# Kernel optimization log

Hardware: AMD Instinct MI355X
Metric: run time of the kernel (lower is better)

The kernel has to match this reference:

```python
import jax, jax.numpy as jnp
import numpy as np

B, N, NFEAT, NHID, NHEADS, NBLK = 8, 512, 32, 128, 4, 6


def _lrelu(x):
    return jax.nn.leaky_relu(x, 0.01)


def _layernorm(x, eps=1e-5):
    m = jnp.mean(x, axis=-1, keepdims=True)
    v = jnp.mean((x - m) ** 2, axis=-1, keepdims=True)
    return (x - m) / jnp.sqrt(v + eps)


def _gat(x, W, a, mask, concat):
    # x:[b,n,f]  W:[H,f,o]  a:[H,2o]  mask:[b,n,n] bool
    o = W.shape[-1]
    Wh = jnp.einsum('bnf,hfo->hbno', x, W)
    s1 = jnp.einsum('hbno,ho->hbn', Wh, a[:, :o])   # Wh @ a[:o]
    s2 = jnp.einsum('hbno,ho->hbn', Wh, a[:, o:])   # Wh @ a[o:]
    # rank-1 score: e[i,j] = leakyrelu(s1[i]*s2[j])
    e = _lrelu(s1[:, :, :, None] * s2[:, :, None, :])  # [h,b,n,n]
    e = jnp.where(mask[None], e, jnp.float32(-9e15))
    att = jax.nn.softmax(e, axis=-1)
    att = jnp.where(mask[None], att, jnp.float32(0.0))
    hp = jnp.einsum('hbij,hbjo->hbio', att, Wh)
    return jax.nn.elu(hp) if concat else hp


def _attn_block(x, W, a, rW, rb, mask):
    res = x
    h = _gat(x, W, a, mask, True)                      # [H,b,n,o]
    h = jnp.moveaxis(h, 0, 2).reshape(x.shape[0], x.shape[1], -1)  # concat heads
    h = h @ rW + rb
    if h.shape[-1] == res.shape[-1]:
        h = h + res
    return _layernorm(h)


def _fel(x, f1w1, f1b1, f1w2, f1b2, f2w1, f2b1, f2w2, f2b2, f3w1, f3b1, f3w2, f3b2):
    res = _lrelu(_lrelu(x @ f1w1 + f1b1) @ f1w2 + f1b2)
    h = _lrelu(_lrelu(res @ f2w1 + f2b1) @ f2w2 + f2b2)
    x = _layernorm(h + res)
    res = x
    h = _lrelu(res @ f3w1 + f3b1) @ f3w2 + f3b2
    return _layernorm(h + res)


def setup_inputs() -> dict:
    key = jax.random.key(0)
    ks = iter(jax.random.split(key, 24))
    nrm = lambda shape: jax.random.normal(next(ks), shape, jnp.float32) * 0.05
    inp = {}
    inp['x'] = jax.random.normal(next(ks), (B, N, NFEAT), jnp.float32)
    inp['adj'] = jax.random.randint(next(ks), (B, N, N), 0, 2, jnp.int32)
    inp['layer_id'] = 0
    inp['f1w1'] = nrm((NFEAT, NHID)); inp['f1b1'] = jnp.zeros((NHID,), jnp.float32)
    inp['f1w2'] = nrm((NHID, NHID)); inp['f1b2'] = jnp.zeros((NHID,), jnp.float32)
    inp['f2w1'] = nrm((NHID, 2 * NHID)); inp['f2b1'] = jnp.zeros((2 * NHID,), jnp.float32)
    inp['f2w2'] = nrm((2 * NHID, NHID)); inp['f2b2'] = jnp.zeros((NHID,), jnp.float32)
    inp['f3w1'] = nrm((NHID, 2 * NHID)); inp['f3b1'] = jnp.zeros((2 * NHID,), jnp.float32)
    inp['f3w2'] = nrm((2 * NHID, NHID)); inp['f3b2'] = jnp.zeros((NHID,), jnp.float32)
    inp['att_W'] = nrm((NBLK, NHEADS, NHID, NHID))
    inp['att_a'] = nrm((NBLK, NHEADS, 2 * NHID))
    inp['resh_W'] = nrm((NBLK, NHEADS * NHID, NHID))
    inp['resh_b'] = jnp.zeros((NBLK, NHID), jnp.float32)
    inp['out_W'] = nrm((2, NHID, NHID))
    inp['out_a'] = nrm((2, 2 * NHID))
    inp['proj_W'] = nrm((2 * NHID, 1))
    inp['proj_b'] = jnp.zeros((1,), jnp.float32)
    return inp


def reference(x, adj, layer_id, f1w1, f1b1, f1w2, f1b2, f2w1, f2b1, f2w2, f2b2,
              f3w1, f3b1, f3w2, f3b2, att_W, att_a, resh_W, resh_b, out_W, out_a,
              proj_W, proj_b):
    mask = adj > 0
    mask_t = jnp.transpose(adj, (0, 2, 1)) > 0
    h = _fel(x, f1w1, f1b1, f1w2, f1b2, f2w1, f2b1, f2w2, f2b2, f3w1, f3b1, f3w2, f3b2)
    for i in range(3):
        h = _attn_block(h, att_W[i], att_a[i], resh_W[i], resh_b[i], mask)
    h = _lrelu(_gat(h, out_W[0:1], out_a[0:1], mask, False)[0])
    ht = h
    for i in range(3, 6):
        ht = _attn_block(ht, att_W[i], att_a[i], resh_W[i], resh_b[i], mask_t)
    ht = _lrelu(_gat(ht, out_W[1:2], out_a[1:2], mask_t, False)[0])
    z = jnp.concatenate([h, ht], axis=-1)   # [b,n,2*nhid]
    z = jnp.mean(z, axis=1)                 # sum/length
    return jnp.squeeze(z @ proj_W + proj_b, axis=1)
```

## Files before the change

kernel.cpp:

```cpp
#include <hip/hip_runtime.h>
#include <math.h>

#define B 8
#define N 512
#define D 128
#define H 4
#define TOK (B*N)

typedef __attribute__((ext_vector_type(8))) short bfrag;
typedef __attribute__((ext_vector_type(4))) float facc;
typedef unsigned short u16;
typedef unsigned int u32;

__device__ __forceinline__ float lrelu(float x){ return x > 0.f ? x : 0.01f*x; }
__device__ __forceinline__ u16 f2bf(float f){
  u32 u = __float_as_uint(f);
  u += 0x7fffu + ((u >> 16) & 1u);
  return (u16)(u >> 16);
}
__device__ __forceinline__ u32 pk2(float a, float b){
  return (u32)f2bf(a) | ((u32)f2bf(b) << 16);
}

#define LS 72

__global__ void prep_kernel(const int* __restrict__ adj,
    u32* __restrict__ mbits, u32* __restrict__ mtbits,
    const float* s0, const float* s1_, const float* s2_, const float* s3,
    const float* s4, const float* s5, const float* s6, const float* s7,
    const float* s8,
    u16* d0, u16* d1, u16* d2, u16* d3, u16* d4, u16* d5, u16* d6, u16* d7, u16* d8)
{
  __shared__ float ftile[32][33];
  const int tid = threadIdx.x;
  const int tx = tid & 31, ty = tid >> 5;
  if (blockIdx.x < 128){
    int* it = (int*)&ftile[0][0];
    const int b = blockIdx.x >> 4, i0 = (blockIdx.x & 15)*32;
    const int lane6 = tid & 63;
    for (int j0 = 0; j0 < N; j0 += 32){
      for (int r = ty; r < 32; r += 8)
        it[r*33 + tx] = adj[((size_t)b*N + i0 + r)*N + j0 + tx];
      __syncthreads();
      #pragma unroll
      for (int half = 0; half < 4; ++half){
        const int r = half*8 + (tid >> 5);
        const int c = tid & 31;
        unsigned long long bl = __ballot(it[r*33 + c] > 0);
        if (lane6 == 0 || lane6 == 32)
          mbits[((size_t)b*N + i0 + r)*16 + (j0>>5)] = (u32)(lane6 ? (bl >> 32) : bl);
        unsigned long long bt = __ballot(it[c*33 + r] > 0);
        if (lane6 == 0 || lane6 == 32)
          mtbits[((size_t)b*N + j0 + r)*16 + (i0>>5)] = (u32)(lane6 ? (bt >> 32) : bt);
      }
      __syncthreads();
    }
  } else {
    const float* srcs[9] = {s0,s1_,s2_,s3,s4,s5,s6,s7,s8};
    u16* dsts[9] = {d0,d1,d2,d3,d4,d5,d6,d7,d8};
    const int Ks[9] = {32,128,128,256,128,256,128,128,512};
    const int Ns[9] = {128,128,256,128,256,128,128,128,128};
    const int zs[9] = {1,1,1,1,1,1,24,2,6};
    for (int job = (int)blockIdx.x - 128; job < 948; job += 384){
      int m = 0, base = 0;
      for (; m < 9; ++m){
        int cnt = (Ks[m]>>5)*(Ns[m]>>5)*zs[m];
        if (job < base + cnt) break;
        base += cnt;
      }
      const int rem = job - base;
      const int tn = Ns[m] >> 5;
      const int per = (Ks[m] >> 5)*tn;
      const int z = rem / per, t = rem % per;
      const int k0 = (t / tn)*32, n0 = (t % tn)*32;
      const float* src = srcs[m] + (size_t)z*Ks[m]*Ns[m];
      u16* dst = dsts[m] + (size_t)z*Ks[m]*Ns[m];
      __syncthreads();
      for (int r = ty; r < 32; r += 8)
        ftile[r][tx] = src[(size_t)(k0+r)*Ns[m] + n0 + tx];
      __syncthreads();
      for (int r = ty; r < 32; r += 8)
        dst[(size_t)(n0+r)*Ks[m] + k0 + tx] = f2bf(ftile[tx][r]);
    }
  }
}

__device__ __forceinline__ void stageB64(const u16* __restrict__ BTn, int ldb,
                                         int k0, u16* Bs, int tid){
  const int n = tid >> 1, part = tid & 1;
  const u16* wp = BTn + (size_t)n*ldb + k0 + part*32;
  uint4 w0 = *(const uint4*)wp,      w1 = *(const uint4*)(wp+8);
  uint4 w2 = *(const uint4*)(wp+16), w3 = *(const uint4*)(wp+24);
  *(uint4*)&Bs[n*LS + part*32]      = w0;
  *(uint4*)&Bs[n*LS + part*32 + 8]  = w1;
  *(uint4*)&Bs[n*LS + part*32 + 16] = w2;
  *(uint4*)&Bs[n*LS + part*32 + 24] = w3;
}
__device__ __forceinline__ void stageB32(const u16* __restrict__ BTn, int ldb,
                                         int k0, u16* Bs, int tid){
  const int n = tid >> 1, part = tid & 1;
  const u16* wp = BTn + (size_t)n*ldb + k0 + part*16;
  uint4 w0 = *(const uint4*)wp, w1 = *(const uint4*)(wp+8);
  *(uint4*)&Bs[n*LS + part*16]     = w0;
  *(uint4*)&Bs[n*LS + part*16 + 8] = w1;
}

__device__ __forceinline__ void mfma64(const u16* As, const u16* Bs,
                                       facc acc[4], int r0, int c0,
                                       int quad, int l15){
  #pragma unroll
  for (int kk = 0; kk < 2; ++kk){
    bfrag af = *(const bfrag*)&As[(r0 + l15)*LS + kk*32 + quad*8];
    #pragma unroll
    for (int g = 0; g < 4; ++g){
      bfrag bf = *(const bfrag*)&Bs[(c0 + g*16 + l15)*LS + kk*32 + quad*8];
      acc[g] = __builtin_amdgcn_mfma_f32_16x16x32_bf16(af, bf, acc[g], 0,0,0);
    }
  }
}
__device__ __forceinline__ void mfma32(const u16* As, const u16* Bs,
                                       facc acc[4], int r0, int c0,
                                       int quad, int l15){
  bfrag af = *(const bfrag*)&As[(r0 + l15)*LS + quad*8];
  #pragma unroll
  for (int g = 0; g < 4; ++g){
    bfrag bf = *(const bfrag*)&Bs[(c0 + g*16 + l15)*LS + quad*8];
    acc[g] = __builtin_amdgcn_mfma_f32_16x16x32_bf16(af, bf, acc[g], 0,0,0);
  }
}

__device__ __forceinline__ void mfma64w(const u16* As, const u16* Bs,
                                        facc acc[2][2], int c0,
                                        int quad, int l15){
  #pragma unroll
  for (int kk = 0; kk < 2; ++kk){
    bfrag af0 = *(const bfrag*)&As[(l15)*LS      + kk*32 + quad*8];
    bfrag af1 = *(const bfrag*)&As[(16 + l15)*LS + kk*32 + quad*8];
    #pragma unroll
    for (int f = 0; f < 2; ++f){
      bfrag bf = *(const bfrag*)&Bs[(c0 + f*16 + l15)*LS + kk*32 + quad*8];
      acc[0][f] = __builtin_amdgcn_mfma_f32_16x16x32_bf16(af0, bf, acc[0][f], 0,0,0);
      acc[1][f] = __builtin_amdgcn_mfma_f32_16x16x32_bf16(af1, bf, acc[1][f], 0,0,0);
    }
  }
}

template<int ACT, int FIN>
__global__ __launch_bounds__(256) void gemm32(
    const float* __restrict__ A, int lda, int K,
    const u16* __restrict__ BT, const float* __restrict__ bias,
    const float* __restrict__ res, float* __restrict__ out, int ldo)
{
  const int tid = threadIdx.x;
  const int t0 = blockIdx.x * 32;
  const int n0 = blockIdx.y * 128;
  __shared__ __align__(16) u16 As[32*LS];
  __shared__ __align__(16) u16 Bs[128*LS];
  __shared__ float scrS[4][16], scrQ[4][16];
  const int wave = tid >> 6, lane = tid & 63, quad = lane >> 4, l15 = lane & 15;
  const int r0 = (wave & 1)*16, c0 = (wave >> 1)*64;
  facc acc[4];
  #pragma unroll
  for (int g = 0; g < 4; ++g) acc[g] = (facc){0.f,0.f,0.f,0.f};
  const u16* BTn = BT + (size_t)n0*K;

  int k0 = 0;
  for (; k0 + 64 <= K; k0 += 64){
    { const int row = tid >> 3, ko = tid & 7;
      const float* ap = A + (size_t)(t0+row)*lda + k0 + ko*8;
      float4 a0 = *(const float4*)ap, a1 = *(const float4*)(ap+4);
      uint4 u = { pk2(a0.x,a0.y), pk2(a0.z,a0.w), pk2(a1.x,a1.y), pk2(a1.z,a1.w) };
      *(uint4*)&As[row*LS + ko*8] = u;
    }
    stageB64(BTn, K, k0, Bs, tid);
    __syncthreads();
    mfma64(As, Bs, acc, r0, c0, quad, l15);
    __syncthreads();
  }
  if (k0 < K){
    { const int row = tid >> 3, ko = tid & 7;
      float4 a0 = *(const float4*)(A + (size_t)(t0+row)*lda + k0 + ko*4);
      uint2 u = { pk2(a0.x,a0.y), pk2(a0.z,a0.w) };
      *(uint2*)&As[row*LS + ko*4] = u;
    }
    stageB32(BTn, K, k0, Bs, tid);
    __syncthreads();
    mfma32(As, Bs, acc, r0, c0, quad, l15);
    __syncthreads();
  }

  float bv[4];
  #pragma unroll
  for (int g = 0; g < 4; ++g) bv[g] = bias[n0 + c0 + g*16 + l15];

  if (FIN == 0){
    #pragma unroll
    for (int g = 0; g < 4; ++g){
      const int c = n0 + c0 + g*16 + l15;
      #pragma unroll
      for (int q = 0; q < 4; ++q){
        const int rq = t0 + r0 + quad*4 + q;
        float xv = acc[g][q] + bv[g];
        if (ACT) xv = lrelu(xv);
        out[(size_t)rq*ldo + c] = xv;
      }
    }
  } else {
    float v[4][4], s[4] = {0,0,0,0}, sq[4] = {0,0,0,0};
    #pragma unroll
    for (int g = 0; g < 4; ++g){
      const int c = c0 + g*16 + l15;
      #pragma unroll
      for (int q = 0; q < 4; ++q){
        const int rq = t0 + r0 + quad*4 + q;
        float xv = acc[g][q] + bv[g];
        if (ACT) xv = lrelu(xv);
        xv += res[(size_t)rq*128 + c];
        v[g][q] = xv; s[q] += xv; sq[q] += xv*xv;
      }
    }
    #pragma unroll
    for (int m = 1; m < 16; m <<= 1){
      #pragma unroll
      for (int q = 0; q < 4; ++q){ s[q] += __shfl_xor(s[q], m, 64); sq[q] += __shfl_xor(sq[q], m, 64); }
    }
    if (l15 == 0){
      #pragma unroll
      for (int q = 0; q < 4; ++q){ scrS[wave][quad*4+q] = s[q]; scrQ[wave][quad*4+q] = sq[q]; }
    }
    __syncthreads();
    #pragma unroll
    for (int q = 0; q < 4; ++q){
      const int rq = t0 + r0 + quad*4 + q;
      const float fs = s[q] + scrS[wave^2][quad*4+q];
      const float fq = sq[q] + scrQ[wave^2][quad*4+q];
      const float mean = fs*(1.f/D);
      const float rstd = rsqrtf(fq*(1.f/D) - mean*mean + 1e-5f);
      #pragma unroll
      for (int g = 0; g < 4; ++g)
        out[(size_t)rq*128 + c0 + g*16 + l15] = (v[g][q] - mean)*rstd;
    }
  }
}

__global__ __launch_bounds__(256) void gemm32b(
    const u16* __restrict__ A, int lda, int K,
    const u16* __restrict__ BT, const float* __restrict__ bias,
    const float* __restrict__ res, float* __restrict__ out)
{
  const int tid = threadIdx.x;
  const int t0 = blockIdx.x * 32;
  __shared__ __align__(16) u16 As[2][32*LS];
  __shared__ __align__(16) u16 Bs[2][128*LS];
  __shared__ float scrS[4][32], scrQ[4][32];
  const int wave = tid >> 6, lane = tid & 63, quad = lane >> 4, l15 = lane & 15;
  const int c0 = wave*32;
  facc acc[2][2];
  #pragma unroll
  for (int rg = 0; rg < 2; ++rg)
    #pragma unroll
    for (int f = 0; f < 2; ++f) acc[rg][f] = (facc){0.f,0.f,0.f,0.f};

  const int arow = tid >> 3, ako = tid & 7;
  const u16* aptr = A + (size_t)(t0+arow)*lda + ako*8;
  const int bn = tid >> 1, bpart = tid & 1;
  const u16* bptr = BT + (size_t)bn*K + bpart*32;

  { uint4 ga = *(const uint4*)aptr;
    uint4 g0 = *(const uint4*)bptr,      g1 = *(const uint4*)(bptr+8);
    uint4 g2 = *(const uint4*)(bptr+16), g3 = *(const uint4*)(bptr+24);
    *(uint4*)&As[0][arow*LS + ako*8] = ga;
    u16* bp = &Bs[0][bn*LS + bpart*32];
    *(uint4*)bp = g0; *(uint4*)(bp+8) = g1; *(uint4*)(bp+16) = g2; *(uint4*)(bp+24) = g3;
  }
  __syncthreads();

  const int nt = K >> 6;
  for (int k = 0; k < nt - 1; ++k){
    const int cur = k & 1, nxt = cur ^ 1;
    uint4 na = *(const uint4*)(aptr + (k+1)*64);
    const u16* wp = bptr + (k+1)*64;
    uint4 n0 = *(const uint4*)wp,      n1 = *(const uint4*)(wp+8);
    uint4 n2 = *(const uint4*)(wp+16), n3 = *(const uint4*)(wp+24);
    mfma64w(As[cur], Bs[cur], acc, c0, quad, l15);
    *(uint4*)&As[nxt][arow*LS + ako*8] = na;
    { u16* bp = &Bs[nxt][bn*LS + bpart*32];
      *(uint4*)bp = n0; *(uint4*)(bp+8) = n1; *(uint4*)(bp+16) = n2; *(uint4*)(bp+24) = n3; }
    __syncthreads();
  }
  mfma64w(As[(nt-1)&1], Bs[(nt-1)&1], acc, c0, quad, l15);

  float bv[2];
  #pragma unroll
  for (int f = 0; f < 2; ++f) bv[f] = bias[c0 + f*16 + l15];
  float v[2][2][4], s[2][4], sq[2][4];
  #pragma unroll
  for (int rg = 0; rg < 2; ++rg)
    #pragma unroll
    for (int q = 0; q < 4; ++q){ s[rg][q] = 0.f; sq[rg][q] = 0.f; }
  #pragma unroll
  for (int rg = 0; rg < 2; ++rg){
    #pragma unroll
    for (int f = 0; f < 2; ++f){
      const int c = c0 + f*16 + l15;
      #pragma unroll
      for (int q = 0; q < 4; ++q){
        const int rq = t0 + rg*16 + quad*4 + q;
        float xv = acc[rg][f][q] + bv[f] + res[(size_t)rq*128 + c];
        v[rg][f][q] = xv; s[rg][q] += xv; sq[rg][q] += xv*xv;
      }
    }
  }
  #pragma unroll
  for (int m = 1; m < 16; m <<= 1){
    #pragma unroll
    for (int rg = 0; rg < 2; ++rg)
      #pragma unroll
      for (int q = 0; q < 4; ++q){ s[rg][q] += __shfl_xor(s[rg][q], m, 64); sq[rg][q] += __shfl_xor(sq[rg][q], m, 64); }
  }
  if (l15 == 0){
    #pragma unroll
    for (int rg = 0; rg < 2; ++rg)
      #pragma unroll
      for (int q = 0; q < 4; ++q){
        scrS[wave][rg*16 + quad*4 + q] = s[rg][q];
        scrQ[wave][rg*16 + quad*4 + q] = sq[rg][q];
      }
  }
  __syncthreads();
  #pragma unroll
  for (int rg = 0; rg < 2; ++rg){
    #pragma unroll
    for (int q = 0; q < 4; ++q){
      const int row = rg*16 + quad*4 + q;
      const float fs = scrS[0][row] + scrS[1][row] + scrS[2][row] + scrS[3][row];
      const float fq = scrQ[0][row] + scrQ[1][row] + scrQ[2][row] + scrQ[3][row];
      const float mean = fs*(1.f/D);
      const float rstd = rsqrtf(fq*(1.f/D) - mean*mean + 1e-5f);
      #pragma unroll
      for (int f = 0; f < 2; ++f)
        out[(size_t)(t0+row)*128 + c0 + f*16 + l15] = (v[rg][f][q] - mean)*rstd;
    }
  }
}

__global__ __launch_bounds__(256) void wh32(
    const float* __restrict__ hin, const u16* __restrict__ WT,
    const float* __restrict__ a, u16* __restrict__ WhT,
    float* __restrict__ s1, float* __restrict__ s2)
{
  const int tid = threadIdx.x;
  const int h  = blockIdx.x >> 7;
  const int t0 = (blockIdx.x & 127) * 32;
  const int b = t0 >> 9, j0 = t0 & (N-1);
  __shared__ __align__(16) u16 As[32*LS];
  __shared__ __align__(16) u16 Bs[128*LS];
  __shared__ float r1s[2][32], r2s[2][32];
  const int wave = tid >> 6, lane = tid & 63, quad = lane >> 4, l15 = lane & 15;
  const int r0 = (wave & 1)*16, c0 = (wave >> 1)*64;
  facc acc[4];
  #pragma unroll
  for (int g = 0; g < 4; ++g) acc[g] = (facc){0.f,0.f,0.f,0.f};
  const u16* BTn = WT + (size_t)h*D*D;

  #pragma unroll
  for (int k0 = 0; k0 < D; k0 += 64){
    { const int row = tid >> 3, ko = tid & 7;
      const float* ap = hin + (size_t)(t0+row)*D + k0 + ko*8;
      float4 a0 = *(const float4*)ap, a1 = *(const float4*)(ap+4);
      uint4 u = { pk2(a0.x,a0.y), pk2(a0.z,a0.w), pk2(a1.x,a1.y), pk2(a1.z,a1.w) };
      *(uint4*)&As[row*LS + ko*8] = u;
    }
    stageB64(BTn, D, k0, Bs, tid);
    __syncthreads();
    mfma64(As, Bs, acc, r0, c0, quad, l15);
    __syncthreads();
  }

  const float* ah = a + (size_t)h*2*D;
  const size_t obase = (size_t)(h*8 + b)*128;
  float p1[4] = {0,0,0,0}, p2[4] = {0,0,0,0};
  #pragma unroll
  for (int g = 0; g < 4; ++g){
    const int c = c0 + g*16 + l15;
    const float a1v = ah[c], a2v = ah[D + c];
    ushort4 wv;
    wv.x = f2bf(acc[g][0]); wv.y = f2bf(acc[g][1]);
    wv.z = f2bf(acc[g][2]); wv.w = f2bf(acc[g][3]);
    *(ushort4*)&WhT[(obase + c)*N + j0 + r0 + quad*4] = wv;
    #pragma unroll
    for (int q = 0; q < 4; ++q){
      p1[q] = fmaf(acc[g][q], a1v, p1[q]);
      p2[q] = fmaf(acc[g][q], a2v, p2[q]);
    }
  }
  #pragma unroll
  for (int m = 1; m < 16; m <<= 1){
    #pragma unroll
    for (int q = 0; q < 4; ++q){ p1[q] += __shfl_xor(p1[q], m, 64); p2[q] += __shfl_xor(p2[q], m, 64); }
  }
  if (l15 == 0){
    #pragma unroll
    for (int q = 0; q < 4; ++q){
      r1s[wave>>1][r0 + quad*4 + q] = p1[q];
      r2s[wave>>1][r0 + quad*4 + q] = p2[q];
    }
  }
  __syncthreads();
  if (tid < 32){
    s1[(size_t)h*TOK + t0 + tid] = r1s[0][tid] + r1s[1][tid];
    s2[(size_t)h*TOK + t0 + tid] = r2s[0][tid] + r2s[1][tid];
  }
}

__device__ __forceinline__ float score8(const float* s2s, const unsigned char* mrow,
                                        float s1lr, int k0, int lq, u16* asp){
  float4 sa = *(const float4*)&s2s[k0 + lq*8];
  float4 sb = *(const float4*)&s2s[k0 + lq*8 + 4];
  const u32 mm = mrow[(k0 >> 3) + lq];
  float ss[8] = {sa.x,sa.y,sa.z,sa.w,sb.x,sb.y,sb.z,sb.w};
  float v[8]; float p = 0.f;
  #pragma unroll
  for (int i = 0; i < 8; ++i){
    float e = lrelu(s1lr * ss[i]);
    float ex = ((mm >> i) & 1u) ? __expf(e) : 0.f;
    v[i] = ex; p += ex;
  }
  uint4 u = { pk2(v[0],v[1]), pk2(v[2],v[3]), pk2(v[4],v[5]), pk2(v[6],v[7]) };
  *(uint4*)asp = u;
  return p;
}

template<int MODE, int OBF>
__global__ __launch_bounds__(256) void pv32(
    const float* __restrict__ s1, const float* __restrict__ s2,
    const u32* __restrict__ mbits, const u16* __restrict__ WhT,
    void* __restrict__ out_, int ldo, int hcs)
{
  const int tid = threadIdx.x;
  const int h  = blockIdx.x >> 7;
  const int t0 = (blockIdx.x & 127) * 32;
  const int b = t0 >> 9, i0 = t0 & (N-1);
  __shared__ float s2s[N];
  __shared__ float s1s[32], sums[32];
  __shared__ u32 mbs[32*16];
  __shared__ __align__(16) u16 As[2][32*LS];
  __shared__ __align__(16) u16 Bs[2][128*LS];

  s2s[tid]     = s2[(size_t)h*TOK + b*N + tid];
  s2s[tid+256] = s2[(size_t)h*TOK + b*N + tid + 256];
  if (tid < 32) s1s[tid] = s1[(size_t)h*TOK + t0 + tid];
  { const int r = tid >> 3, wd = (tid & 7)*2;
    *(uint2*)&mbs[r*16 + wd] = *(const uint2*)&mbits[((size_t)b*N + i0 + r)*16 + wd];
  }

  const u16* BTn = WhT + (size_t)(h*8 + b)*128*N;
  const int wave = tid >> 6, lane = tid & 63, quad = lane >> 4, l15 = lane & 15;
  const int c0 = wave*32;
  facc acc[2][2];
  #pragma unroll
  for (int rg = 0; rg < 2; ++rg)
    #pragma unroll
    for (int f = 0; f < 2; ++f) acc[rg][f] = (facc){0.f,0.f,0.f,0.f};

  const int lr = tid >> 3, lq = tid & 7;
  const unsigned char* mrow = (const unsigned char*)&mbs[lr*16];
  const int bn = tid >> 1, bpart = tid & 1;
  const u16* bwp = BTn + (size_t)bn*N + bpart*32;
  float psum = 0.f;

  uint4 g0 = *(const uint4*)bwp,      g1 = *(const uint4*)(bwp+8);
  uint4 g2 = *(const uint4*)(bwp+16), g3 = *(const uint4*)(bwp+24);
  __syncthreads();
  const float s1lr = s1s[lr];
  psum += score8(s2s, mrow, s1lr, 0, lq, &As[0][lr*LS + lq*8]);
  { u16* bp = &Bs[0][bn*LS + bpart*32];
    *(uint4*)bp = g0; *(uint4*)(bp+8) = g1; *(uint4*)(bp+16) = g2; *(uint4*)(bp+24) = g3; }
  __syncthreads();

  #pragma unroll
  for (int k = 0; k < 7; ++k){
    const int cur = k & 1, nxt = cur ^ 1;
    const u16* wp = bwp + (k+1)*64;
    uint4 n0 = *(const uint4*)wp,      n1 = *(const uint4*)(wp+8);
    uint4 n2 = *(const uint4*)(wp+16), n3 = *(const uint4*)(wp+24);
    psum += score8(s2s, mrow, s1lr, (k+1)*64, lq, &As[nxt][lr*LS + lq*8]);
    mfma64w(As[cur], Bs[cur], acc, c0, quad, l15);
    { u16* bp = &Bs[nxt][bn*LS + bpart*32];
      *(uint4*)bp = n0; *(uint4*)(bp+8) = n1; *(uint4*)(bp+16) = n2; *(uint4*)(bp+24) = n3; }
    __syncthreads();
  }
  mfma64w(As[1], Bs[1], acc, c0, quad, l15);

  #pragma unroll
  for (int m = 1; m < 8; m <<= 1) psum += __shfl_xor(psum, m, 64);
  if (lq == 0) sums[lr] = psum;
  __syncthreads();

  #pragma unroll
  for (int rg = 0; rg < 2; ++rg){
    #pragma unroll
    for (int q = 0; q < 4; ++q){
      const int row = rg*16 + quad*4 + q;
      const float sv = sums[row];
      const float inv = sv > 0.f ? 1.f/sv : 0.f;
      const int rq = t0 + row;
      #pragma unroll
      for (int f = 0; f < 2; ++f){
        float xv = acc[rg][f][q] * inv;
        xv = (MODE == 0) ? (xv > 0.f ? xv : __expf(xv) - 1.f) : lrelu(xv);
        const size_t idx = (size_t)rq*ldo + h*hcs + c0 + f*16 + l15;
        if (OBF) ((u16*)out_)[idx] = f2bf(xv);
        else     ((float*)out_)[idx] = xv;
      }
    }
  }
}

__global__ void final_kernel(const float* __restrict__ hF, const float* __restrict__ hT,
                             const float* __restrict__ pW, const float* __restrict__ pb,
                             float* __restrict__ out)
{
  const int b = blockIdx.x, c = threadIdx.x;
  __shared__ float scr[4];
  const float* src = (c < D) ? (hF + (size_t)b*N*D + c) : (hT + (size_t)b*N*D + (c - D));
  float s = 0.f;
  for (int n = 0; n < N; ++n) s += src[(size_t)n*D];
  s *= (1.f/N);
  float p = s * pW[c];
  #pragma unroll
  for (int m = 32; m; m >>= 1) p += __shfl_xor(p, m, 64);
  __syncthreads();
  if ((c & 63) == 0) scr[c >> 6] = p;
  __syncthreads();
  if (c == 0) out[b] = scr[0] + scr[1] + scr[2] + scr[3] + pb[0];
}

extern "C" void kernel_launch(void* const* d_in, const int* in_sizes, int n_in,
                              void* d_out, int out_size, void* d_ws, size_t ws_size,
                              hipStream_t stream)
{
  (void)in_sizes; (void)n_in; (void)out_size; (void)ws_size;
  const float* x    = (const float*)d_in[0];
  const int*   adj  = (const int*)d_in[1];
  const float* f1w1 = (const float*)d_in[3];
  const float* f1b1 = (const float*)d_in[4];
  const float* f1w2 = (const float*)d_in[5];
  const float* f1b2 = (const float*)d_in[6];
  const float* f2w1 = (const float*)d_in[7];
  const float* f2b1 = (const float*)d_in[8];
  const float* f2w2 = (const float*)d_in[9];
  const float* f2b2 = (const float*)d_in[10];
  const float* f3w1 = (const float*)d_in[11];
  const float* f3b1 = (const float*)d_in[12];
  const float* f3w2 = (const float*)d_in[13];
  const float* f3b2 = (const float*)d_in[14];
  const float* attW = (const float*)d_in[15];
  const float* attA = (const float*)d_in[16];
  const float* rshW = (const float*)d_in[17];
  const float* rshB = (const float*)d_in[18];
  const float* outW = (const float*)d_in[19];
  const float* outA = (const float*)d_in[20];
  const float* pW   = (const float*)d_in[21];
  const float* pb   = (const float*)d_in[22];

  char* w = (char*)d_ws;
  float* hA  = (float*)w; w += (size_t)TOK*128*4;
  float* hB  = (float*)w; w += (size_t)TOK*128*4;
  float* hF  = (float*)w; w += (size_t)TOK*128*4;
  float* hq  = (float*)w; w += (size_t)TOK*256*4;
  u16*  hp2  = (u16*)w;  w += (size_t)TOK*512*2;
  u16*  WhT  = (u16*)w;  w += (size_t)H*8*128*N*2;
  float* s1  = (float*)w; w += (size_t)H*TOK*4;
  float* s2  = (float*)w; w += (size_t)H*TOK*4;
  u32* mbits = (u32*)w;  w += (size_t)B*N*16*4;
  u32* mtbits= (u32*)w;  w += (size_t)B*N*16*4;
  u16* f1w1T = (u16*)w; w += 128*32*2;
  u16* f1w2T = (u16*)w; w += 128*128*2;
  u16* f2w1T = (u16*)w; w += 256*128*2;
  u16* f2w2T = (u16*)w; w += 128*256*2;
  u16* f3w1T = (u16*)w; w += 256*128*2;
  u16* f3w2T = (u16*)w; w += 128*256*2;
  u16* attWT = (u16*)w; w += (size_t)24*128*128*2;
  u16* outWT = (u16*)w; w += (size_t)2*128*128*2;
  u16* rshWT = (u16*)w; w += (size_t)6*128*512*2;

  prep_kernel<<<512,256,0,stream>>>(adj, mbits, mtbits,
      f1w1, f1w2, f2w1, f2w2, f3w1, f3w2, attW, outW, rshW,
      f1w1T, f1w2T, f2w1T, f2w2T, f3w1T, f3w2T, attWT, outWT, rshWT);

  gemm32<1,0><<<dim3(128,1),256,0,stream>>>(x,   32, 32,  f1w1T, f1b1, nullptr, hF, 128);
  gemm32<1,0><<<dim3(128,1),256,0,stream>>>(hF, 128, 128, f1w2T, f1b2, nullptr, hB, 128);
  gemm32<1,0><<<dim3(128,2),256,0,stream>>>(hB, 128, 128, f2w1T, f2b1, nullptr, hq, 256);
  gemm32<1,1><<<dim3(128,1),256,0,stream>>>(hq, 256, 256, f2w2T, f2b2, hB, hF, 128);
  gemm32<1,0><<<dim3(128,2),256,0,stream>>>(hF, 128, 128, f3w1T, f3b1, nullptr, hq, 256);
  gemm32<0,1><<<dim3(128,1),256,0,stream>>>(hq, 256, 256, f3w2T, f3b2, hF, hA, 128);

  float* cur = hA; float* nxt = hB;
  for (int i = 0; i < 3; ++i){
    wh32<<<H*128,256,0,stream>>>(cur, attWT + (size_t)i*H*D*D,
                                 attA + (size_t)i*H*2*D, WhT, s1, s2);
    pv32<0,1><<<H*128,256,0,stream>>>(s1, s2, mbits, WhT, hp2, 512, 128);
    gemm32b<<<128,256,0,stream>>>(hp2, 512, 512,
        rshWT + (size_t)i*128*512, rshB + (size_t)i*D, cur, nxt);
    float* t_ = cur; cur = nxt; nxt = t_;
  }
  wh32<<<128,256,0,stream>>>(cur, outWT, outA, WhT, s1, s2);
  pv32<1,0><<<128,256,0,stream>>>(s1, s2, mbits, WhT, hF, 128, 0);

  cur = hF; nxt = hA;
  for (int i = 3; i < 6; ++i){
    wh32<<<H*128,256,0,stream>>>(cur, attWT + (size_t)i*H*D*D,
                                 attA + (size_t)i*H*2*D, WhT, s1, s2);
    pv32<0,1><<<H*128,256,0,stream>>>(s1, s2, mtbits, WhT, hp2, 512, 128);
    gemm32b<<<128,256,0,stream>>>(hp2, 512, 512,
        rshWT + (size_t)i*128*512, rshB + (size_t)i*D, cur, nxt);
    cur = nxt; nxt = (cur == hA) ? hB : hA;
  }
  wh32<<<128,256,0,stream>>>(cur, outWT + 128*128, outA + 2*D, WhT, s1, s2);
  pv32<1,0><<<128,256,0,stream>>>(s1, s2, mtbits, WhT, nxt, 128, 0);

  final_kernel<<<B,2*D,0,stream>>>(hF, nxt, pW, pb, (float*)d_out);
}
```

Measured before the change: 366.0 us.

## Double-buffer GEMM LDS tiles and widen prep kernel parallelism

The gemm32 and wh32 kernels now keep two LDS buffers, so the global loads for the next K tile are issued before the MFMA on the current tile and only one barrier is needed per step. The prep kernel is relaunched with one block per 64x64 adjacency tile, using int4 loads and 64-bit ballots, plus one block per weight-transpose job, which removes the serial per-block loops. The cost is twice the LDS per block, which can lower occupancy, and an extra barrier was added before the layernorm scratch write so the reused shared memory stays safe.

```diff
diff --git a/kernel.cpp b/kernel.cpp
--- a/kernel.cpp
+++ b/kernel.cpp
@@ -11,6 +11,7 @@
 typedef __attribute__((ext_vector_type(4))) float facc;
 typedef unsigned short u16;
 typedef unsigned int u32;
+typedef unsigned long long u64;
 
 __device__ __forceinline__ float lrelu(float x){ return x > 0.f ? x : 0.01f*x; }
 __device__ __forceinline__ u16 f2bf(float f){
@@ -31,57 +32,58 @@
     const float* s8,
     u16* d0, u16* d1, u16* d2, u16* d3, u16* d4, u16* d5, u16* d6, u16* d7, u16* d8)
 {
-  __shared__ float ftile[32][33];
+  __shared__ int smem[64*65];
   const int tid = threadIdx.x;
-  const int tx = tid & 31, ty = tid >> 5;
-  if (blockIdx.x < 128){
-    int* it = (int*)&ftile[0][0];
-    const int b = blockIdx.x >> 4, i0 = (blockIdx.x & 15)*32;
-    const int lane6 = tid & 63;
-    for (int j0 = 0; j0 < N; j0 += 32){
-      for (int r = ty; r < 32; r += 8)
-        it[r*33 + tx] = adj[((size_t)b*N + i0 + r)*N + j0 + tx];
-      __syncthreads();
-      #pragma unroll
-      for (int half = 0; half < 4; ++half){
-        const int r = half*8 + (tid >> 5);
-        const int c = tid & 31;
-        unsigned long long bl = __ballot(it[r*33 + c] > 0);
-        if (lane6 == 0 || lane6 == 32)
-          mbits[((size_t)b*N + i0 + r)*16 + (j0>>5)] = (u32)(lane6 ? (bl >> 32) : bl);
-        unsigned long long bt = __ballot(it[c*33 + r] > 0);
-        if (lane6 == 0 || lane6 == 32)
-          mtbits[((size_t)b*N + j0 + r)*16 + (i0>>5)] = (u32)(lane6 ? (bt >> 32) : bt);
-      }
-      __syncthreads();
+  if (blockIdx.x < 512){
+    const int tb = blockIdx.x;
+    const int b = tb >> 6, i0 = ((tb >> 3) & 7)*64, j0 = (tb & 7)*64;
+    #pragma unroll
+    for (int i = 0; i < 4; ++i){
+      const int r = i*16 + (tid >> 4);
+      const int c = (tid & 15)*4;
+      int4 v = *(const int4*)&adj[((size_t)b*N + i0 + r)*N + j0 + c];
+      smem[r*65 + c]     = v.x; smem[r*65 + c + 1] = v.y;
+      smem[r*65 + c + 2] = v.z; smem[r*65 + c + 3] = v.w;
+    }
+    __syncthreads();
+    const int wv = tid >> 6, lane = tid & 63;
+    #pragma unroll
+    for (int q = 0; q < 16; ++q){
+      const int r = wv*16 + q;
+      u64 bf_ = __ballot(smem[r*65 + lane] > 0);
+      if (lane == 0)
+        *(u64*)&mbits[((size_t)b*N + i0 + r)*16 + (j0 >> 5)] = bf_;
+      u64 bt_ = __ballot(smem[lane*65 + r] > 0);
+      if (lane == 0)
+        *(u64*)&mtbits[((size_t)b*N + j0 + r)*16 + (i0 >> 5)] = bt_;
     }
   } else {
+    float* ftile = (float*)smem;
+    const int tx = tid & 31, ty = tid >> 5;
     const float* srcs[9] = {s0,s1_,s2_,s3,s4,s5,s6,s7,s8};
     u16* dsts[9] = {d0,d1,d2,d3,d4,d5,d6,d7,d8};
     const int Ks[9] = {32,128,128,256,128,256,128,128,512};
     const int Ns[9] = {128,128,256,128,256,128,128,128,128};
     const int zs[9] = {1,1,1,1,1,1,24,2,6};
-    for (int job = (int)blockIdx.x - 128; job < 948; job += 384){
-      int m = 0, base = 0;
-      for (; m < 9; ++m){
-        int cnt = (Ks[m]>>5)*(Ns[m]>>5)*zs[m];
-        if (job < base + cnt) break;
-        base += cnt;
-      }
-      const int rem = job - base;
-      const int tn = Ns[m] >> 5;
-      const int per = (Ks[m] >> 5)*tn;
-      const int z = rem / per, t = rem % per;
-      const int k0 = (t / tn)*32, n0 = (t % tn)*32;
-      const float* src = srcs[m] + (size_t)z*Ks[m]*Ns[m];
-      u16* dst = dsts[m] + (size_t)z*Ks[m]*Ns[m];
-      __syncthreads();
-      for (int r = ty; r < 32; r += 8)
-        ftile[r][tx] = src[(size_t)(k0+r)*Ns[m] + n0 + tx];
-      __syncthreads();
-      for (int r = ty; r < 32; r += 8)
-        dst[(size_t)(n0+r)*Ks[m] + k0 + tx] = f2bf(ftile[tx][r]);
-    }
+    const int job = (int)blockIdx.x - 512;
+    int m = 0, base = 0;
+    for (; m < 9; ++m){
+      int cnt = (Ks[m]>>5)*(Ns[m]>>5)*zs[m];
+      if (job < base + cnt) break;
+      base += cnt;
+    }
+    const int rem = job - base;
+    const int tn = Ns[m] >> 5;
+    const int per = (Ks[m] >> 5)*tn;
+    const int z = rem / per, t = rem % per;
+    const int k0 = (t / tn)*32, n0 = (t % tn)*32;
+    const float* src = srcs[m] + (size_t)z*Ks[m]*Ns[m];
+    u16* dst = dsts[m] + (size_t)z*Ks[m]*Ns[m];
+    for (int r = ty; r < 32; r += 8)
+      ftile[r*33 + tx] = src[(size_t)(k0+r)*Ns[m] + n0 + tx];
+    __syncthreads();
+    for (int r = ty; r < 32; r += 8)
+      dst[(size_t)(n0+r)*Ks[m] + k0 + tx] = f2bf(ftile[tx*33 + r]);
   }
 }
 
@@ -154,8 +156,8 @@
   const int tid = threadIdx.x;
   const int t0 = blockIdx.x * 32;
   const int n0 = blockIdx.y * 128;
-  __shared__ __align__(16) u16 As[32*LS];
-  __shared__ __align__(16) u16 Bs[128*LS];
+  __shared__ __align__(16) u16 As[2][32*LS];
+  __shared__ __align__(16) u16 Bs[2][128*LS];
   __shared__ float scrS[4][16], scrQ[4][16];
   const int wave = tid >> 6, lane = tid & 63, quad = lane >> 4, l15 = lane & 15;
   const int r0 = (wave & 1)*16, c0 = (wave >> 1)*64;
@@ -164,29 +166,52 @@
   for (int g = 0; g < 4; ++g) acc[g] = (facc){0.f,0.f,0.f,0.f};
   const u16* BTn = BT + (size_t)n0*K;
 
-  int k0 = 0;
-  for (; k0 + 64 <= K; k0 += 64){
-    { const int row = tid >> 3, ko = tid & 7;
-      const float* ap = A + (size_t)(t0+row)*lda + k0 + ko*8;
+  const int arow = tid >> 3, ako = tid & 7;
+  const float* aptr = A + (size_t)(t0+arow)*lda;
+  const int bn = tid >> 1, bpart = tid & 1;
+  const u16* bptr = BTn + (size_t)bn*K;
+
+  const int nt = K >> 6;
+  int kfin = 0;
+  if (nt > 0){
+    { const float* ap = aptr + ako*8;
       float4 a0 = *(const float4*)ap, a1 = *(const float4*)(ap+4);
       uint4 u = { pk2(a0.x,a0.y), pk2(a0.z,a0.w), pk2(a1.x,a1.y), pk2(a1.z,a1.w) };
-      *(uint4*)&As[row*LS + ko*8] = u;
-    }
-    stageB64(BTn, K, k0, Bs, tid);
-    __syncthreads();
-    mfma64(As, Bs, acc, r0, c0, quad, l15);
-    __syncthreads();
-  }
-  if (k0 < K){
-    { const int row = tid >> 3, ko = tid & 7;
-      float4 a0 = *(const float4*)(A + (size_t)(t0+row)*lda + k0 + ko*4);
+      *(uint4*)&As[0][arow*LS + ako*8] = u;
+      const u16* wp = bptr + bpart*32;
+      uint4 g0 = *(const uint4*)wp,      g1 = *(const uint4*)(wp+8);
+      uint4 g2 = *(const uint4*)(wp+16), g3 = *(const uint4*)(wp+24);
+      u16* bp = &Bs[0][bn*LS + bpart*32];
+      *(uint4*)bp = g0; *(uint4*)(bp+8) = g1; *(uint4*)(bp+16) = g2; *(uint4*)(bp+24) = g3;
+    }
+    __syncthreads();
+    for (int k = 0; k < nt - 1; ++k){
+      const int cur = k & 1, nxt = cur ^ 1;
+      const float* ap = aptr + (k+1)*64 + ako*8;
+      float4 a0 = *(const float4*)ap, a1 = *(const float4*)(ap+4);
+      const u16* wp = bptr + (k+1)*64 + bpart*32;
+      uint4 n0v = *(const uint4*)wp,      n1v = *(const uint4*)(wp+8);
+      uint4 n2v = *(const uint4*)(wp+16), n3v = *(const uint4*)(wp+24);
+      mfma64(As[cur], Bs[cur], acc, r0, c0, quad, l15);
+      { uint4 u = { pk2(a0.x,a0.y), pk2(a0.z,a0.w), pk2(a1.x,a1.y), pk2(a1.z,a1.w) };
+        *(uint4*)&As[nxt][arow*LS + ako*8] = u;
+        u16* bp = &Bs[nxt][bn*LS + bpart*32];
+        *(uint4*)bp = n0v; *(uint4*)(bp+8) = n1v; *(uint4*)(bp+16) = n2v; *(uint4*)(bp+24) = n3v; }
+      __syncthreads();
+    }
+    kfin = (nt-1) & 1;
+    mfma64(As[kfin], Bs[kfin], acc, r0, c0, quad, l15);
+  }
+  if (K & 63){
+    if (nt > 0) __syncthreads();
+    const int k0 = nt*64;
+    { float4 a0 = *(const float4*)(aptr + k0 + ako*4);
       uint2 u = { pk2(a0.x,a0.y), pk2(a0.z,a0.w) };
-      *(uint2*)&As[row*LS + ko*4] = u;
-    }
-    stageB32(BTn, K, k0, Bs, tid);
-    __syncthreads();
-    mfma32(As, Bs, acc, r0, c0, quad, l15);
-    __syncthreads();
+      *(uint2*)&As[kfin][arow*LS + ako*4] = u;
+    }
+    stageB32(BTn, K, k0, Bs[kfin], tid);
+    __syncthreads();
+    mfma32(As[kfin], Bs[kfin], acc, r0, c0, quad, l15);
   }
 
   float bv[4];
@@ -224,6 +249,7 @@
       #pragma unroll
       for (int q = 0; q < 4; ++q){ s[q] += __shfl_xor(s[q], m, 64); sq[q] += __shfl_xor(sq[q], m, 64); }
     }
+    __syncthreads();
     if (l15 == 0){
       #pragma unroll
       for (int q = 0; q < 4; ++q){ scrS[wave][quad*4+q] = s[q]; scrQ[wave][quad*4+q] = sq[q]; }
@@ -353,29 +379,40 @@
   const int h  = blockIdx.x >> 7;
   const int t0 = (blockIdx.x & 127) * 32;
   const int b = t0 >> 9, j0 = t0 & (N-1);
-  __shared__ __align__(16) u16 As[32*LS];
-  __shared__ __align__(16) u16 Bs[128*LS];
+  __shared__ __align__(16) u16 As[2][32*LS];
+  __shared__ __align__(16) u16 Bs[2][128*LS];
   __shared__ float r1s[2][32], r2s[2][32];
   const int wave = tid >> 6, lane = tid & 63, quad = lane >> 4, l15 = lane & 15;
   const int r0 = (wave & 1)*16, c0 = (wave >> 1)*64;
   facc acc[4];
   #pragma unroll
   for (int g = 0; g < 4; ++g) acc[g] = (facc){0.f,0.f,0.f,0.f};
-  const u16* BTn = WT + (size_t)h*D*D;
-
-  #pragma unroll
-  for (int k0 = 0; k0 < D; k0 += 64){
-    { const int row = tid >> 3, ko = tid & 7;
-      const float* ap = hin + (size_t)(t0+row)*D + k0 + ko*8;
-      float4 a0 = *(const float4*)ap, a1 = *(const float4*)(ap+4);
-      uint4 u = { pk2(a0.x,a0.y), pk2(a0.z,a0.w), pk2(a1.x,a1.y), pk2(a1.z,a1.w) };
-      *(uint4*)&As[row*LS + ko*8] = u;
-    }
-    stageB64(BTn, D, k0, Bs, tid);
-    __syncthreads();
-    mfma64(As, Bs, acc, r0, c0, quad, l15);
-    __syncthreads();
-  }
+
+  const int arow = tid >> 3, ako = tid & 7;
+  const float* aptr = hin + (size_t)(t0+arow)*D + ako*8;
+  const int bn = tid >> 1, bpart = tid & 1;
+  const u16* bwp = WT + (size_t)h*D*D + (size_t)bn*D + bpart*32;
+
+  { float4 a0 = *(const float4*)aptr, a1 = *(const float4*)(aptr+4);
+    uint4 u = { pk2(a0.x,a0.y), pk2(a0.z,a0.w), pk2(a1.x,a1.y), pk2(a1.z,a1.w) };
+    *(uint4*)&As[0][arow*LS + ako*8] = u;
+    uint4 g0 = *(const uint4*)bwp,      g1 = *(const uint4*)(bwp+8);
+    uint4 g2 = *(const uint4*)(bwp+16), g3 = *(const uint4*)(bwp+24);
+    u16* bp = &Bs[0][bn*LS + bpart*32];
+    *(uint4*)bp = g0; *(uint4*)(bp+8) = g1; *(uint4*)(bp+16) = g2; *(uint4*)(bp+24) = g3;
+  }
+  __syncthreads();
+  { float4 a0 = *(const float4*)(aptr+64), a1 = *(const float4*)(aptr+68);
+    uint4 g0 = *(const uint4*)(bwp+64),    g1 = *(const uint4*)(bwp+72);
+    uint4 g2 = *(const uint4*)(bwp+80),    g3 = *(const uint4*)(bwp+88);
+    mfma64(As[0], Bs[0], acc, r0, c0, quad, l15);
+    uint4 u = { pk2(a0.x,a0.y), pk2(a0.z,a0.w), pk2(a1.x,a1.y), pk2(a1.z,a1.w) };
+    *(uint4*)&As[1][arow*LS + ako*8] = u;
+    u16* bp = &Bs[1][bn*LS + bpart*32];
+    *(uint4*)bp = g0; *(uint4*)(bp+8) = g1; *(uint4*)(bp+16) = g2; *(uint4*)(bp+24) = g3;
+  }
+  __syncthreads();
+  mfma64(As[1], Bs[1], acc, r0, c0, quad, l15);
 
   const float* ah = a + (size_t)h*2*D;
   const size_t obase = (size_t)(h*8 + b)*128;
@@ -585,7 +622,7 @@
   u16* outWT = (u16*)w; w += (size_t)2*128*128*2;
   u16* rshWT = (u16*)w; w += (size_t)6*128*512*2;
 
-  prep_kernel<<<512,256,0,stream>>>(adj, mbits, mtbits,
+  prep_kernel<<<1460,256,0,stream>>>(adj, mbits, mtbits,
       f1w1, f1w2, f2w1, f2w2, f3w1, f3w2, attW, outW, rshW,
       f1w1T, f1w2T, f2w1T, f2w2T, f3w1T, f3w2T, attWT, outWT, rshWT);
 
```

New measurement: 333.9 us. -8.8%, faster.
